# Kernel optimization log

Hardware: AMD Instinct MI355X
Metric: run time of the kernel (lower is better)

The kernel has to match this reference:

```python
import jax, jax.numpy as jnp
import numpy as np

SEQ_LEN = 512
NUM_FEATURES = 16
BATCH = 8
D_MODEL = 512
TOP_K = 5
MAX_P = 512  # largest patch size == seq_len
LAMBD = 0.01


def get_patch_sizes(seq_len):
    # torch: 1/rfftfreq(L)[1:], floor, unique (desc), [::-1] -> ascending unique periods
    freqs = np.fft.rfftfreq(seq_len)[1:]
    periods = np.floor(1.0 / freqs).astype(np.int64)
    return [int(p) for p in np.unique(periods)]


def _sinusoid(n, d):
    pos = np.arange(n, dtype=np.float64)[:, None]
    i = np.arange(d, dtype=np.float64)[None, :]
    angle = pos / np.power(10000.0, (2.0 * np.floor(i / 2.0)) / d)
    return np.where((np.arange(d)[None, :] % 2) == 0, np.sin(angle), np.cos(angle))


def pos_emb_2d(d_model, C, N):
    # 2D sinusoidal positional embedding over (feature idx, patch idx):
    # first half of d_model encodes the feature dim, second half the patch position.
    half = d_model // 2
    pe_feat = _sinusoid(C, half)              # [C, half]
    pe_pos = _sinusoid(N, d_model - half)     # [N, d_model-half]
    pe = np.concatenate([
        np.broadcast_to(pe_feat[:, None, :], (C, N, half)),
        np.broadcast_to(pe_pos[None, :, :], (C, N, d_model - half)),
    ], axis=-1)
    return jnp.asarray(pe, dtype=jnp.float32)  # [C, N, d_model]


def softshrink(x, lambd=LAMBD):
    return jnp.where(x > lambd, x - lambd, jnp.where(x < -lambd, x + lambd, jnp.zeros_like(x)))


def _forward(x, w_start, b_start, w1, b1, w2, b2, w_gate, Wv):
    B, L, C = x.shape
    patch_sizes = get_patch_sizes(L)
    # ---- AFNO1D gating (eval mode: clean logits, no noise) ----
    xs = (x @ w_start)[..., 0] + b_start[0]           # start_fc -> [B, L]
    xf = jnp.fft.rfft(xs, norm='ortho')[:, 1:]        # drop DC -> [B, F], F = L//2
    xr, xi = jnp.real(xf), jnp.imag(xf)
    o1r = jax.nn.relu(xr @ w1[0] - xi @ w1[1] + b1[0])
    o1i = jax.nn.relu(xi @ w1[0] + xr @ w1[1] + b1[1])
    o2r = softshrink(o1r @ w2[0] - o1i @ w2[1] + b2[0])
    o2i = softshrink(o1i @ w2[0] + o1r @ w2[1] + b2[1])
    amp = jnp.sqrt(o2r * o2r + o2i * o2i + 1e-12)     # |complex|, eps for grad safety at 0
    logits = amp @ w_gate                             # [B, E]
    top_w, top_i = jax.lax.top_k(logits, TOP_K)
    top_w = jax.nn.softmax(top_w, axis=-1)
    gates = jnp.zeros_like(logits).at[jnp.arange(B)[:, None], top_i].set(top_w)
    # ---- per-patch-size embedding (dense dispatch: unrouted rows zeroed) ----
    xt = jnp.swapaxes(x, 1, 2)                        # [B, C, L]
    outs = []
    for i, p in enumerate(patch_sizes):               # static loop over 43 experts
        n = -(-L // p)                                # ceil(L / p)
        xp = jnp.pad(xt, ((0, 0), (0, 0), (0, n * p - L)), mode='edge')  # ReplicationPad1d
        patches = xp.reshape(B, C, n, p)              # unfold(-1, p, p)
        emb = jnp.einsum('bcnp,pd->bcnd', patches, Wv[i, :p, :])
        emb = emb + pos_emb_2d(D_MODEL, C, n)[None]
        mask = (gates[:, i] > 0).astype(emb.dtype)
        outs.append(emb * mask[:, None, None, None])
    emb_all = jnp.concatenate(outs, axis=2)           # [B, C, total_patches, d_model]
    return emb_all, gates


def setup_inputs():
    key = jax.random.key(0)
    ks = jax.random.split(key, 8)
    L, C, D = SEQ_LEN, NUM_FEATURES, D_MODEL
    F = L // 2
    E = len(get_patch_sizes(L))
    scale = 1.0 / D
    x = jax.random.normal(ks[0], (BATCH, L, C), jnp.float32)
    w_start = jax.random.normal(ks[1], (C, 1), jnp.float32) / float(np.sqrt(C))
    b_start = jnp.zeros((1,), jnp.float32)
    w1 = scale * jax.random.normal(ks[2], (2, F, 4 * F), jnp.float32)
    b1 = scale * jax.random.normal(ks[3], (2, 4 * F), jnp.float32)
    w2 = scale * jax.random.normal(ks[4], (2, 4 * F, F), jnp.float32)
    b2 = scale * jax.random.normal(ks[5], (2, F), jnp.float32)
    w_gate = 0.01 * jax.random.normal(ks[6], (F, E), jnp.float32)  # randn (not zeros) for nontrivial routing
    Wv = jax.random.normal(ks[7], (E, MAX_P, D), jnp.float32) / float(np.sqrt(MAX_P))  # padded per-expert Linear(p, d_model) weights; expert i uses Wv[i, :p_i]
    return {"x": x, "w_start": w_start, "b_start": b_start, "w1": w1, "b1": b1,
            "w2": w2, "b2": b2, "w_gate": w_gate, "Wv": Wv}


def reference(x, w_start, b_start, w1, b1, w2, b2, w_gate, Wv):
    return _forward(x, w_start, b_start, w1, b1, w2, b2, w_gate, Wv)
```

## Files before the change

### kernel.cpp

```cpp
#include <hip/hip_runtime.h>
#include <math.h>


typedef float v2f __attribute__((ext_vector_type(2)));

constexpr int NEXP = 43;
constexpr int NTOT = 1657;
constexpr long long GATES_OFF = 108593152LL;

constexpr int WS_XR  = 0;
constexpr int WS_XI  = 2048;
constexpr int WS_O1R = 4096;
constexpr int WS_O1I = 12288;
constexpr int WS_LG  = 20480;
constexpr int WS_PEF = 24576;
constexpr int WS_PEP = 28672;

struct Tables {
  int P[NEXP];
  int N[NEXP];
  int SL[NEXP];
  int G0[NEXP];
  int T0[NEXP+1];
  int ne;
};

constexpr Tables make_tables() {
  Tables t{};
  int ne = 0;
  for (int p = 2; p <= 512; ++p) {
    int k = 512 / p;
    if (k >= 1 && k <= 256 && 512 / k == p) { t.P[ne] = p; ++ne; }
  }
  t.ne = ne;
  int g = 0, tl = 0;
  for (int i = 0; i < ne; ++i) {
    int p = t.P[i];
    int n = (512 + p - 1) / p;
    t.N[i] = n;
    int s  = (p >= 512) ? 16 : (p >= 170) ? 8 : (p >= 102) ? 4 : (p >= 64) ? 2 : 1;
    int sl = (s == 16) ? 4 : (s == 8) ? 3 : (s == 4) ? 2 : (s == 2) ? 1 : 0;
    t.SL[i] = sl;
    t.G0[i] = g;  g  += n;
    t.T0[i] = tl; tl += n * s;
  }
  t.T0[ne] = tl;
  return t;
}

constexpr Tables HTBL = make_tables();
static_assert(HTBL.ne == 43, "expert count");
static_assert(HTBL.G0[42] + HTBL.N[42] == 1657, "total patches");
static_assert(HTBL.T0[43] == 1767, "total tiles");

__constant__ Tables TBL = make_tables();

__global__ void k_dft(const float* __restrict__ x, const float* __restrict__ w_start,
                      const float* __restrict__ b_start, float* __restrict__ ws) {
  __shared__ float xs[512];
  int b = blockIdx.x, t = threadIdx.x;
  float w[16];
#pragma unroll
  for (int c = 0; c < 16; ++c) w[c] = w_start[c];
  float bs = b_start[0];
  for (int l = t; l < 512; l += 256) {
    const float* xp = x + ((size_t)b * 512 + l) * 16;
    float s = bs;
#pragma unroll
    for (int c = 0; c < 16; ++c) s = fmaf(xp[c], w[c], s);
    xs[l] = s;
  }
  __syncthreads();
  int k = t + 1;
  float ar = 0.f, ai = 0.f;
  int ph = 0;
  for (int l = 0; l < 512; ++l) {
    float a  = (float)ph * (1.0f / 256.0f);
    float cv = cospif(a), sv = sinpif(a);
    float v  = xs[l];
    ar = fmaf(v,  cv, ar);
    ai = fmaf(-v, sv, ai);
    ph = (ph + k) & 511;
  }
  const float sc = 0.044194173824159216f;
  ws[WS_XR + b * 256 + t] = ar * sc;
  ws[WS_XI + b * 256 + t] = ai * sc;
}

__global__ void k_fc1(const float* __restrict__ w1, const float* __restrict__ b1,
                      float* __restrict__ ws) {
  __shared__ float xr[256], xi[256];
  int b = blockIdx.x >> 2, jg = blockIdx.x & 3, t = threadIdx.x;
  xr[t] = ws[WS_XR + b * 256 + t];
  xi[t] = ws[WS_XI + b * 256 + t];
  __syncthreads();
  int j = jg * 256 + t;
  float s_ra = 0.f, s_rb = 0.f, s_ia = 0.f, s_ib = 0.f;
  for (int k = 0; k < 256; ++k) {
    float a  = w1[k * 1024 + j];
    float bb = w1[262144 + k * 1024 + j];
    float r = xr[k], im = xi[k];
    s_ra = fmaf(r, a, s_ra);  s_ib = fmaf(im, bb, s_ib);
    s_ia = fmaf(im, a, s_ia); s_rb = fmaf(r, bb, s_rb);
  }
  float o1r = s_ra - s_ib + b1[j];
  float o1i = s_ia + s_rb + b1[1024 + j];
  ws[WS_O1R + b * 1024 + j] = fmaxf(o1r, 0.f);
  ws[WS_O1I + b * 1024 + j] = fmaxf(o1i, 0.f);
}

__device__ __forceinline__ float softshrink(float v) {
  const float l = 0.01f;
  return v > l ? v - l : (v < -l ? v + l : 0.f);
}

__global__ void k_fc2(const float* __restrict__ w2, const float* __restrict__ b2,
                      const float* __restrict__ w_gate, float* __restrict__ ws) {
  __shared__ float o1r[1024], o1i[1024], amp[256];
  int b = blockIdx.x, t = threadIdx.x;
  for (int k = t; k < 1024; k += 256) {
    o1r[k] = ws[WS_O1R + b * 1024 + k];
    o1i[k] = ws[WS_O1I + b * 1024 + k];
  }
  __syncthreads();
  float s_rr = 0.f, s_ri = 0.f, s_ir = 0.f, s_ii = 0.f;
  for (int k = 0; k < 1024; ++k) {
    float a  = w2[k * 256 + t];
    float bb = w2[262144 + k * 256 + t];
    float r = o1r[k], im = o1i[k];
    s_rr = fmaf(r, a, s_rr);  s_ii = fmaf(im, bb, s_ii);
    s_ir = fmaf(im, a, s_ir); s_ri = fmaf(r, bb, s_ri);
  }
  float o2r = softshrink(s_rr - s_ii + b2[t]);
  float o2i = softshrink(s_ir + s_ri + b2[256 + t]);
  amp[t] = sqrtf(o2r * o2r + o2i * o2i + 1e-12f);
  __syncthreads();
  if (t < NEXP) {
    float s = 0.f;
    for (int k = 0; k < 256; ++k) s = fmaf(amp[k], w_gate[k * NEXP + t], s);
    ws[WS_LG + b * NEXP + t] = s;
  }
}

__global__ void k_gates(const float* __restrict__ ws, float* __restrict__ out) {
  __shared__ float lg[8][NEXP];
  int t = threadIdx.x;
  for (int z = t; z < 8 * NEXP; z += 64) (&lg[0][0])[z] = ws[WS_LG + z];
  __syncthreads();
  if (t < 8) {
    float vals[5]; int idx[5];
    for (int r = 0; r < 5; ++r) {
      float best = -INFINITY; int bi = 0;
      for (int e = 0; e < NEXP; ++e) {
        float v = lg[t][e];
        if (v > best) { best = v; bi = e; }
      }
      vals[r] = best; idx[r] = bi; lg[t][bi] = -INFINITY;
    }
    float den = 0.f, wv[5];
    for (int r = 0; r < 5; ++r) { wv[r] = expf(vals[r] - vals[0]); den += wv[r]; }
    float g[NEXP];
    for (int e = 0; e < NEXP; ++e) g[e] = 0.f;
    for (int r = 0; r < 5; ++r) g[idx[r]] = wv[r] / den;
    for (int e = 0; e < NEXP; ++e) out[GATES_OFF + (size_t)t * NEXP + e] = g[e];
  }
}

__global__ void k_pe(float* __restrict__ ws) {
  int idx = blockIdx.x * 256 + threadIdx.x;
  const double K = 0.03597789207803196;
  if (idx < 4096) {
    int c = idx >> 8, dd = idx & 255;
    double ang = (double)c * exp(-(double)(dd & ~1) * K);
    ws[WS_PEF + idx] = (float)((dd & 1) ? cos(ang) : sin(ang));
  } else {
    int r = idx - 4096;
    int mm = r >> 8, jj = r & 255;
    double ang = (double)mm * exp(-(double)(jj & ~1) * K);
    ws[WS_PEP + r] = (float)((jj & 1) ? cos(ang) : sin(ang));
  }
}

template <int CPG>
__global__ __launch_bounds__(256)
void k_embed(const float* __restrict__ x, const float* __restrict__ Wv,
             const float* __restrict__ ws, float* __restrict__ out, int tile_base) {
  constexpr int SPLIT = 16 / CPG;
  __shared__ __align__(16) float xl[896];
  int tile = tile_base + blockIdx.x;
  int b = blockIdx.y, t = threadIdx.x;

  int i = 0;
  while (tile >= TBL.T0[i + 1]) ++i;
  int p = TBL.P[i];
  int local = tile - TBL.T0[i];
  int m, cg;
  if (SPLIT == 1) { m = local; cg = 0; }
  else            { m = local / SPLIT; cg = local % SPLIT; }
  int c0 = cg * CPG;
  int g  = TBL.G0[i] + m;
  int d0 = 2 * t;

  float gate = out[GATES_OFF + (size_t)b * NEXP + i];
  size_t obase = (((size_t)(b * 16 + c0) * NTOT) + g) * 512 + d0;
  const size_t cstride = (size_t)NTOT * 512;

  if (gate > 0.f) {
    int tot = p * CPG;
    for (int id = t; id < tot; id += 256) {
      int q = id / CPG, cc = id % CPG;
      int l = m * p + q; l = l > 511 ? 511 : l;
      xl[id] = x[((size_t)b * 512 + l) * 16 + c0 + cc];
    }
    __syncthreads();

    v2f acc[CPG];
#pragma unroll
    for (int cc = 0; cc < CPG; ++cc) { acc[cc].x = 0.f; acc[cc].y = 0.f; }
    const float* wp = Wv + (size_t)i * 262144 + d0;
    for (int q = 0; q < p; ++q) {
      v2f w = *(const v2f*)(wp + (size_t)q * 512);
      const float* xq = xl + q * CPG;
#pragma unroll
      for (int cc = 0; cc < CPG; ++cc) {
        float xv = xq[cc];
        acc[cc].x = fmaf(xv, w.x, acc[cc].x);
        acc[cc].y = fmaf(xv, w.y, acc[cc].y);
      }
    }

    v2f pe[CPG];
    if (d0 < 256) {
#pragma unroll
      for (int cc = 0; cc < CPG; ++cc)
        pe[cc] = *(const v2f*)(ws + WS_PEF + (c0 + cc) * 256 + d0);
    } else {
      v2f pp = *(const v2f*)(ws + WS_PEP + m * 256 + (d0 - 256));
#pragma unroll
      for (int cc = 0; cc < CPG; ++cc) pe[cc] = pp;
    }
#pragma unroll
    for (int cc = 0; cc < CPG; ++cc) {
      v2f v; v.x = acc[cc].x + pe[cc].x; v.y = acc[cc].y + pe[cc].y;
      __builtin_nontemporal_store(v, (v2f*)(out + obase + (size_t)cc * cstride));
    }
  } else {
    v2f z; z.x = 0.f; z.y = 0.f;
#pragma unroll
    for (int cc = 0; cc < CPG; ++cc)
      __builtin_nontemporal_store(z, (v2f*)(out + obase + (size_t)cc * cstride));
  }
}

extern "C" void kernel_launch(void* const* d_in, const int* in_sizes, int n_in,
                              void* d_out, int out_size, void* d_ws, size_t ws_size,
                              hipStream_t stream) {
  const float* x       = (const float*)d_in[0];
  const float* w_start = (const float*)d_in[1];
  const float* b_start = (const float*)d_in[2];
  const float* w1      = (const float*)d_in[3];
  const float* b1      = (const float*)d_in[4];
  const float* w2      = (const float*)d_in[5];
  const float* b2      = (const float*)d_in[6];
  const float* w_gate  = (const float*)d_in[7];
  const float* Wv      = (const float*)d_in[8];
  float* out = (float*)d_out;
  float* ws  = (float*)d_ws;

  k_dft  <<<8,   256, 0, stream>>>(x, w_start, b_start, ws);
  k_fc1  <<<32,  256, 0, stream>>>(w1, b1, ws);
  k_fc2  <<<8,   256, 0, stream>>>(w2, b2, w_gate, ws);
  k_gates<<<1,    64, 0, stream>>>(ws, out);
  k_pe   <<<272, 256, 0, stream>>>(ws);

  int i = 0;
  while (i < NEXP) {
    int sl = HTBL.SL[i];
    int j = i;
    while (j < NEXP && HTBL.SL[j] == sl) ++j;
    int base = HTBL.T0[i];
    int cnt  = HTBL.T0[j] - base;
    dim3 grid(cnt, 8);
    switch (sl) {
      case 0: k_embed<16><<<grid, 256, 0, stream>>>(x, Wv, ws, out, base); break;
      case 1: k_embed<8> <<<grid, 256, 0, stream>>>(x, Wv, ws, out, base); break;
      case 2: k_embed<4> <<<grid, 256, 0, stream>>>(x, Wv, ws, out, base); break;
      case 3: k_embed<2> <<<grid, 256, 0, stream>>>(x, Wv, ws, out, base); break;
      case 4: k_embed<1> <<<grid, 256, 0, stream>>>(x, Wv, ws, out, base); break;
    }
    i = j;
  }
}
```

Baseline: 645.7 us.

## Zero-fill output upfront, skip ungated experts, widen embed tiles, split fc2

Adds a bulk vector zero-fill kernel for the large output. Embedding blocks for ungated experts now return early instead of each writing its own zeros. Embed tiles use float4 loads and stores, with threads split across channels, a constant tile map and a changed split policy. fc2 is split into partial-sum and reduce kernels for more parallelism, gating is fused into fc2b, and the PE computation moves to float and merges into the DFT kernel. The cost is that the whole output is written twice for gated experts, and the positional encoding loses some precision in float.

```diff
diff --git a/kernel.cpp b/kernel.cpp
--- a/kernel.cpp
+++ b/kernel.cpp
@@ -2,89 +2,114 @@
 #include <math.h>
 
 
-typedef float v2f __attribute__((ext_vector_type(2)));
+typedef float v4f __attribute__((ext_vector_type(4)));
 
 constexpr int NEXP = 43;
 constexpr int NTOT = 1657;
 constexpr long long GATES_OFF = 108593152LL;
+constexpr int OUT_V4 = 27148288;
 
 constexpr int WS_XR  = 0;
 constexpr int WS_XI  = 2048;
 constexpr int WS_O1R = 4096;
 constexpr int WS_O1I = 12288;
-constexpr int WS_LG  = 20480;
-constexpr int WS_PEF = 24576;
-constexpr int WS_PEP = 28672;
+constexpr int WS_P2  = 20480;
+constexpr int WS_PEF = 53248;
+constexpr int WS_PEP = 57344;
 
 struct Tables {
-  int P[NEXP];
-  int N[NEXP];
-  int SL[NEXP];
-  int G0[NEXP];
-  int T0[NEXP+1];
-  int ne;
+  int P[NEXP], N[NEXP], SP[NEXP], G0[NEXP], T0[NEXP+1], TB[5], ne;
 };
+constexpr int split_of(int p) { return p >= 170 ? 8 : p >= 102 ? 4 : p >= 64 ? 2 : 1; }
 
 constexpr Tables make_tables() {
   Tables t{};
   int ne = 0;
   for (int p = 2; p <= 512; ++p) {
     int k = 512 / p;
-    if (k >= 1 && k <= 256 && 512 / k == p) { t.P[ne] = p; ++ne; }
+    if (k >= 1 && 512 / k == p) t.P[ne++] = p;
   }
   t.ne = ne;
   int g = 0, tl = 0;
   for (int i = 0; i < ne; ++i) {
-    int p = t.P[i];
-    int n = (512 + p - 1) / p;
-    t.N[i] = n;
-    int s  = (p >= 512) ? 16 : (p >= 170) ? 8 : (p >= 102) ? 4 : (p >= 64) ? 2 : 1;
-    int sl = (s == 16) ? 4 : (s == 8) ? 3 : (s == 4) ? 2 : (s == 2) ? 1 : 0;
-    t.SL[i] = sl;
-    t.G0[i] = g;  g  += n;
-    t.T0[i] = tl; tl += n * s;
+    int p = t.P[i], n = (512 + p - 1) / p;
+    t.N[i] = n; t.SP[i] = split_of(p);
+    t.G0[i] = g;  g += n;
+    t.T0[i] = tl; tl += n * t.SP[i];
   }
   t.T0[ne] = tl;
+  t.TB[0] = 0;
+  for (int l = 0; l < 4; ++l) {
+    int s = (l == 0) ? 1 : (l == 1) ? 2 : (l == 2) ? 4 : 8;
+    int a = 0;
+    for (int i = 0; i < ne; ++i) if (t.SP[i] <= s) a += t.N[i] * t.SP[i];
+    t.TB[l + 1] = a;
+  }
   return t;
 }
-
 constexpr Tables HTBL = make_tables();
 static_assert(HTBL.ne == 43, "expert count");
-static_assert(HTBL.G0[42] + HTBL.N[42] == 1657, "total patches");
-static_assert(HTBL.T0[43] == 1767, "total tiles");
-
-__constant__ Tables TBL = make_tables();
-
-__global__ void k_dft(const float* __restrict__ x, const float* __restrict__ w_start,
+static_assert(HTBL.G0[42] + HTBL.N[42] == NTOT, "total patches");
+static_assert(HTBL.T0[43] == 1759, "total tiles");
+static_assert(HTBL.TB[4] == 1759, "boundaries");
+
+constexpr int NTILE = 1759;
+struct TileMap { int v[NTILE]; };
+constexpr TileMap make_tmap() {
+  TileMap tm{};
+  int idx = 0;
+  for (int i = 0; i < HTBL.ne; ++i)
+    for (int m = 0; m < HTBL.N[i]; ++m)
+      for (int cg = 0; cg < HTBL.SP[i]; ++cg)
+        tm.v[idx++] = i | (m << 6) | (cg << 15);
+  return tm;
+}
+__constant__ TileMap TMAPC = make_tmap();
+__constant__ Tables  TBLC  = make_tables();
+
+__global__ void k_pre(const float* __restrict__ x, const float* __restrict__ w_start,
                       const float* __restrict__ b_start, float* __restrict__ ws) {
-  __shared__ float xs[512];
-  int b = blockIdx.x, t = threadIdx.x;
-  float w[16];
-#pragma unroll
-  for (int c = 0; c < 16; ++c) w[c] = w_start[c];
-  float bs = b_start[0];
-  for (int l = t; l < 512; l += 256) {
-    const float* xp = x + ((size_t)b * 512 + l) * 16;
-    float s = bs;
-#pragma unroll
-    for (int c = 0; c < 16; ++c) s = fmaf(xp[c], w[c], s);
-    xs[l] = s;
-  }
-  __syncthreads();
-  int k = t + 1;
-  float ar = 0.f, ai = 0.f;
-  int ph = 0;
-  for (int l = 0; l < 512; ++l) {
-    float a  = (float)ph * (1.0f / 256.0f);
-    float cv = cospif(a), sv = sinpif(a);
-    float v  = xs[l];
-    ar = fmaf(v,  cv, ar);
-    ai = fmaf(-v, sv, ai);
-    ph = (ph + k) & 511;
-  }
-  const float sc = 0.044194173824159216f;
-  ws[WS_XR + b * 256 + t] = ar * sc;
-  ws[WS_XI + b * 256 + t] = ai * sc;
+  if (blockIdx.x < 8) {
+    __shared__ float xs[512];
+    int b = blockIdx.x, t = threadIdx.x;
+    float w[16];
+#pragma unroll
+    for (int c = 0; c < 16; ++c) w[c] = w_start[c];
+    float bs = b_start[0];
+    for (int l = t; l < 512; l += 256) {
+      const float* xp = x + ((size_t)b * 512 + l) * 16;
+      float s = bs;
+#pragma unroll
+      for (int c = 0; c < 16; ++c) s = fmaf(xp[c], w[c], s);
+      xs[l] = s;
+    }
+    __syncthreads();
+    int k = t + 1;
+    float ar = 0.f, ai = 0.f;
+    int ph = 0;
+    for (int l = 0; l < 512; ++l) {
+      float a = (float)ph * (1.0f / 256.0f);
+      float v = xs[l];
+      ar = fmaf(v,  cospif(a), ar);
+      ai = fmaf(-v, sinpif(a), ai);
+      ph = (ph + k) & 511;
+    }
+    const float sc = 0.044194173824159216f;
+    ws[WS_XR + b * 256 + t] = ar * sc;
+    ws[WS_XI + b * 256 + t] = ai * sc;
+  } else {
+    int idx = (blockIdx.x - 8) * 256 + threadIdx.x;
+    const float K = 0.03597789207803197f;
+    if (idx < 4096) {
+      int c = idx >> 8, d = idx & 255;
+      float ang = (float)c * expf(-(float)(d & ~1) * K);
+      ws[WS_PEF + idx] = (d & 1) ? cosf(ang) : sinf(ang);
+    } else {
+      int r = idx - 4096, mm = r >> 8, j = r & 255;
+      float ang = (float)mm * expf(-(float)(j & ~1) * K);
+      ws[WS_PEP + r] = (j & 1) ? cosf(ang) : sinf(ang);
+    }
+  }
 }
 
 __global__ void k_fc1(const float* __restrict__ w1, const float* __restrict__ b1,
@@ -103,10 +128,27 @@
     s_ra = fmaf(r, a, s_ra);  s_ib = fmaf(im, bb, s_ib);
     s_ia = fmaf(im, a, s_ia); s_rb = fmaf(r, bb, s_rb);
   }
-  float o1r = s_ra - s_ib + b1[j];
-  float o1i = s_ia + s_rb + b1[1024 + j];
-  ws[WS_O1R + b * 1024 + j] = fmaxf(o1r, 0.f);
-  ws[WS_O1I + b * 1024 + j] = fmaxf(o1i, 0.f);
+  ws[WS_O1R + b * 1024 + j] = fmaxf(s_ra - s_ib + b1[j], 0.f);
+  ws[WS_O1I + b * 1024 + j] = fmaxf(s_ia + s_rb + b1[1024 + j], 0.f);
+}
+
+__global__ void k_fc2a(const float* __restrict__ w2, float* __restrict__ ws) {
+  __shared__ float lr[256], li[256];
+  int b = blockIdx.x >> 2, kc = blockIdx.x & 3, t = threadIdx.x;
+  lr[t] = ws[WS_O1R + b * 1024 + kc * 256 + t];
+  li[t] = ws[WS_O1I + b * 1024 + kc * 256 + t];
+  __syncthreads();
+  float s_rr = 0.f, s_ri = 0.f, s_ir = 0.f, s_ii = 0.f;
+  int kb = kc * 256;
+  for (int k = 0; k < 256; ++k) {
+    float a  = w2[(kb + k) * 256 + t];
+    float bb = w2[262144 + (kb + k) * 256 + t];
+    float r = lr[k], im = li[k];
+    s_rr = fmaf(r, a, s_rr);  s_ii = fmaf(im, bb, s_ii);
+    s_ir = fmaf(im, a, s_ir); s_ri = fmaf(r, bb, s_ri);
+  }
+  float* P = ws + WS_P2 + (size_t)(b * 4 + kc) * 1024 + t;
+  P[0] = s_rr; P[256] = s_ii; P[512] = s_ir; P[768] = s_ri;
 }
 
 __device__ __forceinline__ float softshrink(float v) {
@@ -114,22 +156,14 @@
   return v > l ? v - l : (v < -l ? v + l : 0.f);
 }
 
-__global__ void k_fc2(const float* __restrict__ w2, const float* __restrict__ b2,
-                      const float* __restrict__ w_gate, float* __restrict__ ws) {
-  __shared__ float o1r[1024], o1i[1024], amp[256];
+__global__ void k_fc2b(const float* __restrict__ b2, const float* __restrict__ w_gate,
+                       float* __restrict__ ws, float* __restrict__ out) {
+  __shared__ float amp[256], lg[64];
   int b = blockIdx.x, t = threadIdx.x;
-  for (int k = t; k < 1024; k += 256) {
-    o1r[k] = ws[WS_O1R + b * 1024 + k];
-    o1i[k] = ws[WS_O1I + b * 1024 + k];
-  }
-  __syncthreads();
-  float s_rr = 0.f, s_ri = 0.f, s_ir = 0.f, s_ii = 0.f;
-  for (int k = 0; k < 1024; ++k) {
-    float a  = w2[k * 256 + t];
-    float bb = w2[262144 + k * 256 + t];
-    float r = o1r[k], im = o1i[k];
-    s_rr = fmaf(r, a, s_rr);  s_ii = fmaf(im, bb, s_ii);
-    s_ir = fmaf(im, a, s_ir); s_ri = fmaf(r, bb, s_ri);
+  float s_rr = 0.f, s_ii = 0.f, s_ir = 0.f, s_ri = 0.f;
+  for (int kc = 0; kc < 4; ++kc) {
+    const float* P = ws + WS_P2 + (size_t)(b * 4 + kc) * 1024 + t;
+    s_rr += P[0]; s_ii += P[256]; s_ir += P[512]; s_ri += P[768];
   }
   float o2r = softshrink(s_rr - s_ii + b2[t]);
   float o2i = softshrink(s_ir + s_ri + b2[256 + t]);
@@ -138,117 +172,99 @@
   if (t < NEXP) {
     float s = 0.f;
     for (int k = 0; k < 256; ++k) s = fmaf(amp[k], w_gate[k * NEXP + t], s);
-    ws[WS_LG + b * NEXP + t] = s;
-  }
-}
-
-__global__ void k_gates(const float* __restrict__ ws, float* __restrict__ out) {
-  __shared__ float lg[8][NEXP];
-  int t = threadIdx.x;
-  for (int z = t; z < 8 * NEXP; z += 64) (&lg[0][0])[z] = ws[WS_LG + z];
-  __syncthreads();
-  if (t < 8) {
+    lg[t] = s;
+  }
+  __syncthreads();
+  if (t == 0) {
+    float v[NEXP];
+    for (int e = 0; e < NEXP; ++e) v[e] = lg[e];
     float vals[5]; int idx[5];
     for (int r = 0; r < 5; ++r) {
       float best = -INFINITY; int bi = 0;
-      for (int e = 0; e < NEXP; ++e) {
-        float v = lg[t][e];
-        if (v > best) { best = v; bi = e; }
-      }
-      vals[r] = best; idx[r] = bi; lg[t][bi] = -INFINITY;
+      for (int e = 0; e < NEXP; ++e)
+        if (v[e] > best) { best = v[e]; bi = e; }
+      vals[r] = best; idx[r] = bi; v[bi] = -INFINITY;
     }
     float den = 0.f, wv[5];
     for (int r = 0; r < 5; ++r) { wv[r] = expf(vals[r] - vals[0]); den += wv[r]; }
     float g[NEXP];
     for (int e = 0; e < NEXP; ++e) g[e] = 0.f;
     for (int r = 0; r < 5; ++r) g[idx[r]] = wv[r] / den;
-    for (int e = 0; e < NEXP; ++e) out[GATES_OFF + (size_t)t * NEXP + e] = g[e];
-  }
-}
-
-__global__ void k_pe(float* __restrict__ ws) {
-  int idx = blockIdx.x * 256 + threadIdx.x;
-  const double K = 0.03597789207803196;
-  if (idx < 4096) {
-    int c = idx >> 8, dd = idx & 255;
-    double ang = (double)c * exp(-(double)(dd & ~1) * K);
-    ws[WS_PEF + idx] = (float)((dd & 1) ? cos(ang) : sin(ang));
-  } else {
-    int r = idx - 4096;
-    int mm = r >> 8, jj = r & 255;
-    double ang = (double)mm * exp(-(double)(jj & ~1) * K);
-    ws[WS_PEP + r] = (float)((jj & 1) ? cos(ang) : sin(ang));
-  }
+    for (int e = 0; e < NEXP; ++e) out[GATES_OFF + (size_t)b * NEXP + e] = g[e];
+  }
+}
+
+__global__ void k_fill(float* __restrict__ out) {
+  size_t id = (size_t)blockIdx.x * 256 + threadIdx.x;
+  v4f z = {0.f, 0.f, 0.f, 0.f};
+  v4f* o = (v4f*)out;
+#pragma unroll
+  for (int s = 0; s < 8; ++s)
+    o[id + (size_t)s * 3393536] = z;
 }
 
 template <int CPG>
 __global__ __launch_bounds__(256)
 void k_embed(const float* __restrict__ x, const float* __restrict__ Wv,
-             const float* __restrict__ ws, float* __restrict__ out, int tile_base) {
-  constexpr int SPLIT = 16 / CPG;
-  __shared__ __align__(16) float xl[896];
-  int tile = tile_base + blockIdx.x;
-  int b = blockIdx.y, t = threadIdx.x;
-
-  int i = 0;
-  while (tile >= TBL.T0[i + 1]) ++i;
-  int p = TBL.P[i];
-  int local = tile - TBL.T0[i];
-  int m, cg;
-  if (SPLIT == 1) { m = local; cg = 0; }
-  else            { m = local / SPLIT; cg = local % SPLIT; }
+             const float* __restrict__ ws, float* __restrict__ out, int base) {
+  constexpr int CPT = CPG / 2;
+  __shared__ __align__(16) float xl[1024];
+  int tile = base + blockIdx.x, b = blockIdx.y, t = threadIdx.x;
+  int info = TMAPC.v[tile];
+  int i = info & 63, m = (info >> 6) & 511, cg = info >> 15;
+
+  float gate = out[GATES_OFF + (size_t)b * NEXP + i];
+  if (gate <= 0.f) return;
+
+  int p  = TBLC.P[i];
   int c0 = cg * CPG;
-  int g  = TBL.G0[i] + m;
-  int d0 = 2 * t;
-
-  float gate = out[GATES_OFF + (size_t)b * NEXP + i];
-  size_t obase = (((size_t)(b * 16 + c0) * NTOT) + g) * 512 + d0;
+  int g  = TBLC.G0[i] + m;
+  int dg = t & 127, tch = t >> 7;
+  int d0 = dg * 4;
+
+  int tot = p * CPG;
+  for (int id = t; id < tot; id += 256) {
+    int q = id / CPG, cc = id % CPG;
+    int l = m * p + q; l = l > 511 ? 511 : l;
+    xl[id] = x[((size_t)b * 512 + l) * 16 + c0 + cc];
+  }
+  __syncthreads();
+
+  v4f acc[CPT];
+#pragma unroll
+  for (int j = 0; j < CPT; ++j) acc[j] = (v4f){0.f, 0.f, 0.f, 0.f};
+  const float* wp = Wv + (size_t)i * 262144 + d0;
+  const float* xb = xl + tch * CPT;
+  for (int q = 0; q < p; ++q) {
+    v4f w = *(const v4f*)(wp + (size_t)q * 512);
+    const float* xq = xb + q * CPG;
+#pragma unroll
+    for (int j = 0; j < CPT; ++j) {
+      float xv = xq[j];
+      acc[j].x = fmaf(xv, w.x, acc[j].x);
+      acc[j].y = fmaf(xv, w.y, acc[j].y);
+      acc[j].z = fmaf(xv, w.z, acc[j].z);
+      acc[j].w = fmaf(xv, w.w, acc[j].w);
+    }
+  }
+
+  int cA = c0 + tch * CPT;
   const size_t cstride = (size_t)NTOT * 512;
-
-  if (gate > 0.f) {
-    int tot = p * CPG;
-    for (int id = t; id < tot; id += 256) {
-      int q = id / CPG, cc = id % CPG;
-      int l = m * p + q; l = l > 511 ? 511 : l;
-      xl[id] = x[((size_t)b * 512 + l) * 16 + c0 + cc];
-    }
-    __syncthreads();
-
-    v2f acc[CPG];
-#pragma unroll
-    for (int cc = 0; cc < CPG; ++cc) { acc[cc].x = 0.f; acc[cc].y = 0.f; }
-    const float* wp = Wv + (size_t)i * 262144 + d0;
-    for (int q = 0; q < p; ++q) {
-      v2f w = *(const v2f*)(wp + (size_t)q * 512);
-      const float* xq = xl + q * CPG;
-#pragma unroll
-      for (int cc = 0; cc < CPG; ++cc) {
-        float xv = xq[cc];
-        acc[cc].x = fmaf(xv, w.x, acc[cc].x);
-        acc[cc].y = fmaf(xv, w.y, acc[cc].y);
-      }
-    }
-
-    v2f pe[CPG];
-    if (d0 < 256) {
-#pragma unroll
-      for (int cc = 0; cc < CPG; ++cc)
-        pe[cc] = *(const v2f*)(ws + WS_PEF + (c0 + cc) * 256 + d0);
-    } else {
-      v2f pp = *(const v2f*)(ws + WS_PEP + m * 256 + (d0 - 256));
-#pragma unroll
-      for (int cc = 0; cc < CPG; ++cc) pe[cc] = pp;
-    }
-#pragma unroll
-    for (int cc = 0; cc < CPG; ++cc) {
-      v2f v; v.x = acc[cc].x + pe[cc].x; v.y = acc[cc].y + pe[cc].y;
-      __builtin_nontemporal_store(v, (v2f*)(out + obase + (size_t)cc * cstride));
+  size_t obase = (((size_t)(b * 16 + cA) * NTOT) + g) * 512 + d0;
+  if (d0 < 256) {
+#pragma unroll
+    for (int j = 0; j < CPT; ++j) {
+      v4f pe = *(const v4f*)(ws + WS_PEF + (cA + j) * 256 + d0);
+      v4f v = acc[j] + pe;
+      *(v4f*)(out + obase + (size_t)j * cstride) = v;
     }
   } else {
-    v2f z; z.x = 0.f; z.y = 0.f;
-#pragma unroll
-    for (int cc = 0; cc < CPG; ++cc)
-      __builtin_nontemporal_store(z, (v2f*)(out + obase + (size_t)cc * cstride));
+    v4f pe = *(const v4f*)(ws + WS_PEP + m * 256 + (d0 - 256));
+#pragma unroll
+    for (int j = 0; j < CPT; ++j) {
+      v4f v = acc[j] + pe;
+      *(v4f*)(out + obase + (size_t)j * cstride) = v;
+    }
   }
 }
 
@@ -267,27 +283,14 @@
   float* out = (float*)d_out;
   float* ws  = (float*)d_ws;
 
-  k_dft  <<<8,   256, 0, stream>>>(x, w_start, b_start, ws);
+  k_pre  <<<280, 256, 0, stream>>>(x, w_start, b_start, ws);
   k_fc1  <<<32,  256, 0, stream>>>(w1, b1, ws);
-  k_fc2  <<<8,   256, 0, stream>>>(w2, b2, w_gate, ws);
-  k_gates<<<1,    64, 0, stream>>>(ws, out);
-  k_pe   <<<272, 256, 0, stream>>>(ws);
-
-  int i = 0;
-  while (i < NEXP) {
-    int sl = HTBL.SL[i];
-    int j = i;
-    while (j < NEXP && HTBL.SL[j] == sl) ++j;
-    int base = HTBL.T0[i];
-    int cnt  = HTBL.T0[j] - base;
-    dim3 grid(cnt, 8);
-    switch (sl) {
-      case 0: k_embed<16><<<grid, 256, 0, stream>>>(x, Wv, ws, out, base); break;
-      case 1: k_embed<8> <<<grid, 256, 0, stream>>>(x, Wv, ws, out, base); break;
-      case 2: k_embed<4> <<<grid, 256, 0, stream>>>(x, Wv, ws, out, base); break;
-      case 3: k_embed<2> <<<grid, 256, 0, stream>>>(x, Wv, ws, out, base); break;
-      case 4: k_embed<1> <<<grid, 256, 0, stream>>>(x, Wv, ws, out, base); break;
-    }
-    i = j;
-  }
-}
+  k_fc2a <<<32,  256, 0, stream>>>(w2, ws);
+  k_fc2b <<<8,   256, 0, stream>>>(b2, w_gate, ws, out);
+  k_fill <<<13256, 256, 0, stream>>>(out);
+
+  k_embed<16><<<dim3(HTBL.TB[1], 8), 256, 0, stream>>>(x, Wv, ws, out, 0);
+  k_embed<8> <<<dim3(HTBL.TB[2] - HTBL.TB[1], 8), 256, 0, stream>>>(x, Wv, ws, out, HTBL.TB[1]);
+  k_embed<4> <<<dim3(HTBL.TB[3] - HTBL.TB[2], 8), 256, 0, stream>>>(x, Wv, ws, out, HTBL.TB[2]);
+  k_embed<2> <<<dim3(HTBL.TB[4] - HTBL.TB[3], 8), 256, 0, stream>>>(x, Wv, ws, out, HTBL.TB[3]);
+}
```

Result: faster. 605.5 us (-6.2%).
